# Kernel optimization log

Hardware: AMD Instinct MI355X
Metric: run time of the kernel (lower is better)

The kernel has to match this reference:

```python
import jax, jax.numpy as jnp
import numpy as np

DIM = 256
HEADS = 8
WIN = 64
SHIFT = 32
HIDDEN = 1024  # dim * mlp_ratio
EPS = 1e-5


def layernorm(x, g, b):
    mu = jnp.mean(x, axis=-1, keepdims=True)
    var = jnp.mean(jnp.square(x - mu), axis=-1, keepdims=True)
    return (x - mu) * jax.lax.rsqrt(var + EPS) * g + b


def setup_inputs() -> dict:
    key = jax.random.key(0)
    ks = jax.random.split(key, 12)
    B, L = 8, 16384
    s = lambda fan: 1.0 / np.sqrt(fan)
    return {
        "x": jax.random.normal(ks[0], (B, L, DIM), dtype=jnp.float32),
        "g1": jnp.ones((DIM,), jnp.float32),
        "b1": jnp.zeros((DIM,), jnp.float32),
        "qkv_w": jax.random.normal(ks[1], (DIM, 3 * DIM), jnp.float32) * s(DIM),
        "qkv_b": jnp.zeros((3 * DIM,), jnp.float32),
        "rpb_table": jax.random.normal(ks[2], (2 * WIN - 1, HEADS), jnp.float32) * 0.02,
        "proj_w": jax.random.normal(ks[3], (DIM, DIM), jnp.float32) * s(DIM),
        "proj_b": jnp.zeros((DIM,), jnp.float32),
        "g2": jnp.ones((DIM,), jnp.float32),
        "b2": jnp.zeros((DIM,), jnp.float32),
        "fc1_w": jax.random.normal(ks[4], (DIM, HIDDEN), jnp.float32) * s(DIM),
        "fc1_b": jnp.zeros((HIDDEN,), jnp.float32),
        "fc2_w": jax.random.normal(ks[5], (HIDDEN, DIM), jnp.float32) * s(HIDDEN),
        "fc2_b": jnp.zeros((DIM,), jnp.float32),
    }


def reference(x, g1, b1, qkv_w, qkv_b, rpb_table, proj_w, proj_b, g2, b2, fc1_w, fc1_b, fc2_w, fc2_b):
    B, L, C = x.shape
    hd = C // HEADS
    scale = hd ** (-0.5)

    shortcut = x
    xn = layernorm(x, g1, b1)

    # shift: roll left, zero wrapped-around tail (faithful to original in-place zeroing)
    shifted = jnp.roll(xn, -SHIFT, axis=1)
    shifted = shifted.at[:, -SHIFT:].set(0.0)

    nW = L // WIN
    xw = shifted.reshape(B * nW, WIN, C)

    # qkv projection
    qkv = xw @ qkv_w + qkv_b
    qkv = qkv.reshape(-1, WIN, 3, HEADS, hd).transpose(2, 0, 3, 1, 4)
    q, k, v = qkv[0], qkv[1], qkv[2]

    attn = jnp.einsum('bhnd,bhmd->bhnm', q * scale, k)

    idx = jnp.arange(WIN)
    rel = idx[:, None] - idx[None, :] + (WIN - 1)
    bias = rpb_table[rel].transpose(2, 0, 1)
    attn = attn + bias[None]

    attn = jax.nn.softmax(attn, axis=-1)
    out = jnp.einsum('bhnm,bhmd->bhnd', attn, v)
    out = out.transpose(0, 2, 1, 3).reshape(-1, WIN, C)
    out = out @ proj_w + proj_b

    # window reverse + unshift (zero wrapped head, faithful to original)
    xr = out.reshape(B, L, C)
    xr = jnp.roll(xr, SHIFT, axis=1)
    xr = xr.at[:, :SHIFT].set(0.0)

    x1 = shortcut + xr
    h = layernorm(x1, g2, b2)
    h = jax.nn.gelu(h @ fc1_w + fc1_b, approximate=False)
    h = h @ fc2_w + fc2_b
    return x1 + h
```

## Files before the change

### kernel.cpp

```cpp
#include <hip/hip_runtime.h>
#include <hip/hip_bf16.h>
#include <stdint.h>

#define LSEQ   16384
#define NBATCH 8
#define MROWS  (NBATCH*LSEQ)
#define CDIM   256
#define NHEADS 8
#define HDIM   32
#define NWIN   64
#define NSH    32
#define NHID   1024

typedef unsigned short u16;
typedef __attribute__((ext_vector_type(4))) float f32x4;
typedef __attribute__((ext_vector_type(8))) short s16x8;

__device__ __forceinline__ u16 f2bf(float f) {
  union { float f; unsigned u; } c; c.f = f;
  unsigned r = c.u + 0x7FFFu + ((c.u >> 16) & 1u);
  return (u16)(r >> 16);
}

__device__ __forceinline__ float gelu_fast(float v) {
  float t = v * v;
  float u2 = v * fmaf(t, 0.0713548162726f, 1.59576912161f);
  float e = __expf(u2);
  float r = __builtin_amdgcn_rcpf(e + 1.f);
  return fmaf(-v, r, v);
}

__global__ __launch_bounds__(256) void wtrans_kernel(const float* __restrict__ in,
                                                     u16* __restrict__ out, int K, int N) {
  __shared__ float tile[64][65];
  int k0 = blockIdx.x * 64, n0 = blockIdx.y * 64;
  int t = threadIdx.x;
  int r = t >> 4, cb = (t & 15) * 4;
#pragma unroll
  for (int p = 0; p < 4; ++p) {
    const float4 v = *(const float4*)(in + (size_t)(k0 + r + p*16) * N + n0 + cb);
    tile[r+p*16][cb+0] = v.x; tile[r+p*16][cb+1] = v.y;
    tile[r+p*16][cb+2] = v.z; tile[r+p*16][cb+3] = v.w;
  }
  __syncthreads();
#pragma unroll
  for (int p = 0; p < 4; ++p) {
    int nl = r + p*16;
    ushort4 o;
    o.x = f2bf(tile[cb+0][nl]); o.y = f2bf(tile[cb+1][nl]);
    o.z = f2bf(tile[cb+2][nl]); o.w = f2bf(tile[cb+3][nl]);
    *(ushort4*)(out + (size_t)(n0+nl)*K + k0 + cb) = o;
  }
}

__global__ __launch_bounds__(256) void ln_shift_kernel(const float* __restrict__ x,
                                                       const float* __restrict__ g,
                                                       const float* __restrict__ b,
                                                       u16* __restrict__ out) {
  int row  = blockIdx.x * 4 + (threadIdx.x >> 6);
  int lane = threadIdx.x & 63;
  u16* op = out + (size_t)row * CDIM + lane*4;
  int l  = row & (LSEQ-1);
  int ls = l + NSH;
  if (ls >= LSEQ) { *(ushort4*)op = make_ushort4(0,0,0,0); return; }
  const float4 v = *(const float4*)(x + ((size_t)(row - l) + ls) * CDIM + lane*4);
  float s  = v.x+v.y+v.z+v.w;
  float s2 = v.x*v.x + v.y*v.y + v.z*v.z + v.w*v.w;
#pragma unroll
  for (int m = 1; m < 64; m <<= 1) { s += __shfl_xor(s, m); s2 += __shfl_xor(s2, m); }
  float mean = s * (1.f/CDIM);
  float rs = rsqrtf(s2*(1.f/CDIM) - mean*mean + 1e-5f);
  const float4 gv = *(const float4*)(g + lane*4);
  const float4 bv = *(const float4*)(b + lane*4);
  ushort4 o;
  o.x = f2bf((v.x-mean)*rs*gv.x + bv.x);
  o.y = f2bf((v.y-mean)*rs*gv.y + bv.y);
  o.z = f2bf((v.z-mean)*rs*gv.z + bv.z);
  o.w = f2bf((v.w-mean)*rs*gv.w + bv.w);
  *(ushort4*)op = o;
}

template<int KDIM, int NDIM>
__global__ __launch_bounds__(256) void gemm_kernel(const u16* __restrict__ A,
                                                   const u16* __restrict__ BT,
                                                   const float* __restrict__ bias,
                                                   u16* __restrict__ Cout) {
  __shared__ __align__(16) u16 As[128*64];
  __shared__ __align__(16) u16 Bs[128*64];
  const int t = threadIdx.x, wave = t >> 6, lane = t & 63;
  constexpr int NT_N = NDIM / 128;
  constexpr int G = 32;
  const int bid = blockIdx.x;
  const int chunk = bid / (G * NT_N);
  const int rem = bid - chunk * (G * NT_N);
  const int tn = rem / G;
  const int tm = chunk * G + (rem - tn * G);
  f32x4 acc[4][4];
#pragma unroll
  for (int m = 0; m < 4; ++m)
#pragma unroll
    for (int n = 0; n < 4; ++n) acc[m][n] = (f32x4){0.f,0.f,0.f,0.f};

  const size_t Aoff = (size_t)tm * 128 * KDIM;
  const size_t Boff = (size_t)tn * 128 * KDIM;
  int rowS[4], kblkS[4];
#pragma unroll
  for (int p = 0; p < 4; ++p) {
    int i = p*256 + t; rowS[p] = i >> 3;
    kblkS[p] = ((i & 7) ^ (rowS[p] & 7)) * 8;
  }
  const int wr = (wave >> 1) * 64, wc = (wave & 1) * 64;

  for (int kt = 0; kt < KDIM/64; ++kt) {
    const int k0 = kt * 64;
#pragma unroll
    for (int p = 0; p < 4; ++p) {
      __builtin_amdgcn_global_load_lds(
        (const __attribute__((address_space(1))) void*)(A + Aoff + (size_t)rowS[p]*KDIM + k0 + kblkS[p]),
        (__attribute__((address_space(3))) void*)(As + (p*256 + wave*64)*8), 16, 0, 0);
      __builtin_amdgcn_global_load_lds(
        (const __attribute__((address_space(1))) void*)(BT + Boff + (size_t)rowS[p]*KDIM + k0 + kblkS[p]),
        (__attribute__((address_space(3))) void*)(Bs + (p*256 + wave*64)*8), 16, 0, 0);
    }
    asm volatile("s_waitcnt vmcnt(0)" ::: "memory");
    __syncthreads();
#pragma unroll
    for (int kk = 0; kk < 2; ++kk) {
      s16x8 af[4], bf[4];
#pragma unroll
      for (int m = 0; m < 4; ++m) {
        int r = wr + m*16 + (lane & 15);
        int slot = (kk*4 + (lane >> 4)) ^ (r & 7);
        af[m] = *(const s16x8*)&As[r*64 + slot*8];
      }
#pragma unroll
      for (int n = 0; n < 4; ++n) {
        int r = wc + n*16 + (lane & 15);
        int slot = (kk*4 + (lane >> 4)) ^ (r & 7);
        bf[n] = *(const s16x8*)&Bs[r*64 + slot*8];
      }
#pragma unroll
      for (int m = 0; m < 4; ++m)
#pragma unroll
        for (int n = 0; n < 4; ++n)
          acc[m][n] = __builtin_amdgcn_mfma_f32_16x16x32_bf16(bf[n], af[m], acc[m][n], 0, 0, 0);
    }
    __syncthreads();
  }

  const int g = lane >> 4, c0 = lane & 15;
  const size_t row0 = (size_t)tm*128 + wr;
  const int col0 = tn*128 + wc;
  float4 bvv[4];
#pragma unroll
  for (int n = 0; n < 4; ++n) bvv[n] = *(const float4*)(bias + col0 + n*16 + g*4);
#pragma unroll
  for (int m = 0; m < 4; ++m) {
    size_t R = row0 + m*16 + c0;
    u16* orow = Cout + R * NDIM + col0 + g*4;
#pragma unroll
    for (int n = 0; n < 4; ++n) {
      ushort4 o;
      o.x = f2bf(acc[m][n][0] + bvv[n].x);
      o.y = f2bf(acc[m][n][1] + bvv[n].y);
      o.z = f2bf(acc[m][n][2] + bvv[n].z);
      o.w = f2bf(acc[m][n][3] + bvv[n].w);
      *(ushort4*)(orow + n*16) = o;
    }
  }
}

__global__ __launch_bounds__(256) void proj_ln_kernel(const u16* __restrict__ A,
                                                      const u16* __restrict__ BT,
                                                      const float* __restrict__ bias,
                                                      const float* __restrict__ x,
                                                      const float* __restrict__ g2,
                                                      const float* __restrict__ b2,
                                                      float* __restrict__ out,
                                                      u16* __restrict__ ln_out) {
  __shared__ __align__(16) u16 As[64*64];
  __shared__ __align__(16) u16 Bs[256*64];
  const int t = threadIdx.x, wave = t >> 6, lane = t & 63;
  const int g = lane >> 4, c0 = lane & 15;
  const int row0 = blockIdx.x * 64;

  f32x4 acc[16];
#pragma unroll
  for (int n = 0; n < 16; ++n) acc[n] = (f32x4){0.f,0.f,0.f,0.f};

  for (int kt = 0; kt < 4; ++kt) {
    const int k0 = kt * 64;
#pragma unroll
    for (int p = 0; p < 2; ++p) {
      int i = p*256 + t;
      int r = i >> 3;
      int srow = row0 - NSH + r; if (srow < 0) srow = 0;
      int kb = ((i & 7) ^ (r & 7)) * 8;
      __builtin_amdgcn_global_load_lds(
        (const __attribute__((address_space(1))) void*)(A + (size_t)srow*CDIM + k0 + kb),
        (__attribute__((address_space(3))) void*)(As + i*8), 16, 0, 0);
    }
#pragma unroll
    for (int p = 0; p < 8; ++p) {
      int i = p*256 + t;
      int r = i >> 3;
      int kb = ((i & 7) ^ (r & 7)) * 8;
      __builtin_amdgcn_global_load_lds(
        (const __attribute__((address_space(1))) void*)(BT + (size_t)r*CDIM + k0 + kb),
        (__attribute__((address_space(3))) void*)(Bs + i*8), 16, 0, 0);
    }
    asm volatile("s_waitcnt vmcnt(0)" ::: "memory");
    __syncthreads();
#pragma unroll
    for (int kk = 0; kk < 2; ++kk) {
      const int ar = wave*16 + c0;
      s16x8 af = *(const s16x8*)&As[ar*64 + (((kk*4 + g) ^ (ar & 7)) * 8)];
#pragma unroll
      for (int nn = 0; nn < 4; ++nn) {
        s16x8 bf[4];
#pragma unroll
        for (int q = 0; q < 4; ++q) {
          int rn = (nn*4 + q)*16 + c0;
          bf[q] = *(const s16x8*)&Bs[rn*64 + (((kk*4 + g) ^ (rn & 7)) * 8)];
        }
#pragma unroll
        for (int q = 0; q < 4; ++q)
          acc[nn*4+q] = __builtin_amdgcn_mfma_f32_16x16x32_bf16(bf[q], af, acc[nn*4+q], 0, 0, 0);
      }
    }
    __syncthreads();
  }

  const int D = row0 + wave*16 + c0;
  const int l_d = D & (LSEQ-1);
  const bool addp = (l_d >= NSH);
  float s = 0.f, s2 = 0.f;
  f32x4 x1v[16];
#pragma unroll
  for (int n = 0; n < 16; ++n) {
    const int col = n*16 + g*4;
    const float4 xv = *(const float4*)(x + (size_t)D*CDIM + col);
    const float4 bv = *(const float4*)(bias + col);
    f32x4 v;
    v[0] = addp ? xv.x + acc[n][0] + bv.x : xv.x;
    v[1] = addp ? xv.y + acc[n][1] + bv.y : xv.y;
    v[2] = addp ? xv.z + acc[n][2] + bv.z : xv.z;
    v[3] = addp ? xv.w + acc[n][3] + bv.w : xv.w;
    *(f32x4*)(out + (size_t)D*CDIM + col) = v;
    x1v[n] = v;
    s  += v[0]+v[1]+v[2]+v[3];
    s2 += v[0]*v[0]+v[1]*v[1]+v[2]*v[2]+v[3]*v[3];
  }
  s  += __shfl_xor(s, 16);  s  += __shfl_xor(s, 32);
  s2 += __shfl_xor(s2, 16); s2 += __shfl_xor(s2, 32);
  const float mean = s * (1.f/CDIM);
  const float rs = rsqrtf(s2*(1.f/CDIM) - mean*mean + 1e-5f);
#pragma unroll
  for (int n = 0; n < 16; ++n) {
    const int col = n*16 + g*4;
    const float4 gv = *(const float4*)(g2 + col);
    const float4 bv = *(const float4*)(b2 + col);
    ushort4 o;
    o.x = f2bf((x1v[n][0]-mean)*rs*gv.x + bv.x);
    o.y = f2bf((x1v[n][1]-mean)*rs*gv.y + bv.y);
    o.z = f2bf((x1v[n][2]-mean)*rs*gv.z + bv.z);
    o.w = f2bf((x1v[n][3]-mean)*rs*gv.w + bv.w);
    *(ushort4*)(ln_out + (size_t)D*CDIM + col) = o;
  }
}

__global__ __launch_bounds__(256) void mlp_kernel(const u16* __restrict__ A,
                                                  const u16* __restrict__ W1T,
                                                  const u16* __restrict__ W2T,
                                                  const float* __restrict__ b1,
                                                  const float* __restrict__ b2,
                                                  float* __restrict__ out) {
  __shared__ __align__(16) u16 Xs[64*256];
  __shared__ __align__(16) u16 Ws[256*64];
  __shared__ __align__(16) u16 Hs[64*128];
  const int t = threadIdx.x, wave = t >> 6, lane = t & 63;
  const int g = lane >> 4, c0 = lane & 15;
  const int row0 = blockIdx.x * 64;

#pragma unroll
  for (int p = 0; p < 8; ++p) {
    int i = p*256 + t, r = i >> 5, cb = i & 31;
    __builtin_amdgcn_global_load_lds(
      (const __attribute__((address_space(1))) void*)(A + (size_t)(row0 + r)*CDIM + ((cb ^ (r & 7))*8)),
      (__attribute__((address_space(3))) void*)(Xs + i*8), 16, 0, 0);
  }
  f32x4 acc2[4][4];
#pragma unroll
  for (int m = 0; m < 4; ++m)
#pragma unroll
    for (int n = 0; n < 4; ++n) acc2[m][n] = (f32x4){0.f,0.f,0.f,0.f};
  asm volatile("s_waitcnt vmcnt(0)" ::: "memory");
  __syncthreads();

#pragma unroll 1
  for (int hc = 0; hc < 8; ++hc) {
    f32x4 acc1[4][2];
#pragma unroll
    for (int m = 0; m < 4; ++m) { acc1[m][0] = (f32x4){0.f,0.f,0.f,0.f}; acc1[m][1] = (f32x4){0.f,0.f,0.f,0.f}; }
#pragma unroll
    for (int kt = 0; kt < 4; ++kt) {
#pragma unroll
      for (int p = 0; p < 4; ++p) {
        int i = p*256 + t, r = i >> 3, cb = i & 7;
        __builtin_amdgcn_global_load_lds(
          (const __attribute__((address_space(1))) void*)(W1T + (size_t)(hc*128 + r)*256 + kt*64 + ((cb ^ (r & 7))*8)),
          (__attribute__((address_space(3))) void*)(Ws + i*8), 16, 0, 0);
      }
      asm volatile("s_waitcnt vmcnt(0)" ::: "memory");
      __syncthreads();
#pragma unroll
      for (int kk = 0; kk < 2; ++kk) {
        s16x8 af[4], bf[2];
        const int q = kt*2 + kk;
#pragma unroll
        for (int m = 0; m < 4; ++m) {
          int r = m*16 + c0;
          af[m] = *(const s16x8*)&Xs[r*256 + (((q*4 + g) ^ (r & 7))*8)];
        }
#pragma unroll
        for (int n = 0; n < 2; ++n) {
          int rw = wave*32 + n*16 + c0;
          bf[n] = *(const s16x8*)&Ws[rw*64 + (((kk*4 + g) ^ (rw & 7))*8)];
        }
#pragma unroll
        for (int m = 0; m < 4; ++m)
#pragma unroll
          for (int n = 0; n < 2; ++n)
            acc1[m][n] = __builtin_amdgcn_mfma_f32_16x16x32_bf16(bf[n], af[m], acc1[m][n], 0, 0, 0);
      }
      __syncthreads();
    }
    {
      float4 b1v[2];
#pragma unroll
      for (int n = 0; n < 2; ++n) b1v[n] = *(const float4*)(b1 + hc*128 + wave*32 + n*16 + g*4);
#pragma unroll
      for (int m = 0; m < 4; ++m) {
        int r = m*16 + c0;
#pragma unroll
        for (int n = 0; n < 2; ++n) {
          ushort4 o;
          o.x = f2bf(gelu_fast(acc1[m][n][0] + b1v[n].x));
          o.y = f2bf(gelu_fast(acc1[m][n][1] + b1v[n].y));
          o.z = f2bf(gelu_fast(acc1[m][n][2] + b1v[n].z));
          o.w = f2bf(gelu_fast(acc1[m][n][3] + b1v[n].w));
          int colb = wave*4 + n*2 + (g >> 1);
          *(ushort4*)((char*)Hs + r*256 + ((colb ^ (r & 7)) << 4) + (g & 1)*8) = o;
        }
      }
    }
    __syncthreads();
#pragma unroll
    for (int kt2 = 0; kt2 < 2; ++kt2) {
#pragma unroll
      for (int p = 0; p < 8; ++p) {
        int i = p*256 + t, r = i >> 3, cb = i & 7;
        __builtin_amdgcn_global_load_lds(
          (const __attribute__((address_space(1))) void*)(W2T + (size_t)r*NHID + hc*128 + kt2*64 + ((cb ^ (r & 7))*8)),
          (__attribute__((address_space(3))) void*)(Ws + i*8), 16, 0, 0);
      }
      asm volatile("s_waitcnt vmcnt(0)" ::: "memory");
      __syncthreads();
#pragma unroll
      for (int kk = 0; kk < 2; ++kk) {
        s16x8 af[4], bf[4];
        const int s2 = kt2*2 + kk;
#pragma unroll
        for (int m = 0; m < 4; ++m) {
          int r = m*16 + c0;
          af[m] = *(const s16x8*)&Hs[r*128 + (((s2*4 + g) ^ (r & 7))*8)];
        }
#pragma unroll
        for (int n = 0; n < 4; ++n) {
          int rw = wave*64 + n*16 + c0;
          bf[n] = *(const s16x8*)&Ws[rw*64 + (((kk*4 + g) ^ (rw & 7))*8)];
        }
#pragma unroll
        for (int m = 0; m < 4; ++m)
#pragma unroll
          for (int n = 0; n < 4; ++n)
            acc2[m][n] = __builtin_amdgcn_mfma_f32_16x16x32_bf16(bf[n], af[m], acc2[m][n], 0, 0, 0);
      }
      __syncthreads();
    }
  }
  float4 b2v[4];
#pragma unroll
  for (int n = 0; n < 4; ++n) b2v[n] = *(const float4*)(b2 + wave*64 + n*16 + g*4);
#pragma unroll
  for (int m = 0; m < 4; ++m) {
    size_t base = (size_t)(row0 + m*16 + c0)*CDIM + wave*64 + g*4;
#pragma unroll
    for (int n = 0; n < 4; ++n) {
      float4 rv = *(const float4*)(out + base + n*16);
      float4 o;
      o.x = rv.x + acc2[m][n][0] + b2v[n].x;
      o.y = rv.y + acc2[m][n][1] + b2v[n].y;
      o.z = rv.z + acc2[m][n][2] + b2v[n].z;
      o.w = rv.w + acc2[m][n][3] + b2v[n].w;
      *(float4*)(out + base + n*16) = o;
    }
  }
}

__global__ __launch_bounds__(256) void attn_kernel(const u16* __restrict__ qkv,
                                                   const float* __restrict__ rpb,
                                                   u16* __restrict__ out) {
  __shared__ __align__(16) u16 VT[NHEADS*HDIM*NWIN];
  __shared__ __align__(16) u16 Pl[4*NWIN*NWIN];
  __shared__ float biasl[NHEADS][128];
  const int t = threadIdx.x, wave = t >> 6, lane = t & 63;
  const int g = lane >> 4, c0 = lane & 15;
  const size_t rowbase = (size_t)blockIdx.x * NWIN;

  for (int e = t; e < NHEADS*128; e += 256) {
    int h = e >> 7, i = e & 127;
    biasl[h][i] = (i < 2*NWIN-1) ? rpb[i*NHEADS + h] : 0.f;
  }
  {
    int cA = t >> 5;
    int inner = t & 31;
    int hh = inner >> 2, d0 = (inner & 3) * 8;
#pragma unroll
    for (int p = 0; p < 8; ++p) {
      int c = p*8 + cA;
      s16x8 v = *(const s16x8*)&qkv[(rowbase + c)*768 + 512 + hh*32 + d0];
#pragma unroll
      for (int j = 0; j < 8; ++j) {
        int d = d0 + j;
        int slot = (c >> 3) ^ (d & 7) ^ hh;
        *(u16*)((char*)VT + hh*4096 + d*128 + slot*16 + (c & 7)*2) = (u16)v[j];
      }
    }
  }
  __syncthreads();

  const float scale = 0.17677669529663687f;
#pragma unroll 1
  for (int rep = 0; rep < 2; ++rep) {
    const int h = wave*2 + rep;
    s16x8 qf[4], kf[4];
#pragma unroll
    for (int m = 0; m < 4; ++m)
      qf[m] = *(const s16x8*)&qkv[(rowbase + m*16 + c0)*768 + h*32 + g*8];
#pragma unroll
    for (int n = 0; n < 4; ++n)
      kf[n] = *(const s16x8*)&qkv[(rowbase + n*16 + c0)*768 + 256 + h*32 + g*8];
    f32x4 sa[4][4];
#pragma unroll
    for (int m = 0; m < 4; ++m)
#pragma unroll
      for (int n = 0; n < 4; ++n) sa[m][n] = (f32x4){0.f,0.f,0.f,0.f};
#pragma unroll
    for (int m = 0; m < 4; ++m)
#pragma unroll
      for (int n = 0; n < 4; ++n)
        sa[m][n] = __builtin_amdgcn_mfma_f32_16x16x32_bf16(qf[m], kf[n], sa[m][n], 0, 0, 0);
#pragma unroll
    for (int m = 0; m < 4; ++m)
#pragma unroll
      for (int n = 0; n < 4; ++n) {
        int idx0 = (m-n)*16 + 4*g - c0 + 63;
#pragma unroll
        for (int j = 0; j < 4; ++j)
          sa[m][n][j] = sa[m][n][j]*scale + biasl[h][idx0 + j];
      }
    float rm[4][4], rsum[4][4];
#pragma unroll
    for (int m = 0; m < 4; ++m)
#pragma unroll
      for (int j = 0; j < 4; ++j) {
        float mx = fmaxf(fmaxf(sa[m][0][j], sa[m][1][j]), fmaxf(sa[m][2][j], sa[m][3][j]));
        mx = fmaxf(mx, __shfl_xor(mx, 1));
        mx = fmaxf(mx, __shfl_xor(mx, 2));
        mx = fmaxf(mx, __shfl_xor(mx, 4));
        mx = fmaxf(mx, __shfl_xor(mx, 8));
        rm[m][j] = mx;
      }
#pragma unroll
    for (int m = 0; m < 4; ++m)
#pragma unroll
      for (int n = 0; n < 4; ++n)
#pragma unroll
        for (int j = 0; j < 4; ++j)
          sa[m][n][j] = __expf(sa[m][n][j] - rm[m][j]);
#pragma unroll
    for (int m = 0; m < 4; ++m)
#pragma unroll
      for (int j = 0; j < 4; ++j) {
        float s = sa[m][0][j] + sa[m][1][j] + sa[m][2][j] + sa[m][3][j];
        s += __shfl_xor(s, 1);
        s += __shfl_xor(s, 2);
        s += __shfl_xor(s, 4);
        s += __shfl_xor(s, 8);
        rsum[m][j] = 1.f / s;
      }
    asm volatile("s_waitcnt lgkmcnt(0)" ::: "memory");
#pragma unroll
    for (int m = 0; m < 4; ++m)
#pragma unroll
      for (int n = 0; n < 4; ++n)
#pragma unroll
        for (int j = 0; j < 4; ++j) {
          int r = m*16 + 4*g + j, c = n*16 + c0;
          *(u16*)((char*)Pl + wave*8192 + r*128 + (((c>>3)^(r&7))*16) + (c&7)*2)
            = f2bf(sa[m][n][j] * rsum[m][j]);
        }
    asm volatile("s_waitcnt lgkmcnt(0)" ::: "memory");
    __builtin_amdgcn_sched_barrier(0);
    f32x4 oa[4][2];
#pragma unroll
    for (int m = 0; m < 4; ++m) { oa[m][0] = (f32x4){0.f,0.f,0.f,0.f}; oa[m][1] = (f32x4){0.f,0.f,0.f,0.f}; }
#pragma unroll
    for (int kk = 0; kk < 2; ++kk) {
      s16x8 pa[4], vb[2];
#pragma unroll
      for (int m = 0; m < 4; ++m) {
        int r = m*16 + c0;
        int slot = (kk*4 + g) ^ (r & 7);
        pa[m] = *(const s16x8*)((const char*)Pl + wave*8192 + r*128 + slot*16);
      }
#pragma unroll
      for (int n = 0; n < 2; ++n) {
        int d = n*16 + c0;
        int slot = (kk*4 + g) ^ (d & 7) ^ h;
        vb[n] = *(const s16x8*)((const char*)VT + h*4096 + d*128 + slot*16);
      }
#pragma unroll
      for (int m = 0; m < 4; ++m)
#pragma unroll
        for (int n = 0; n < 2; ++n)
          oa[m][n] = __builtin_amdgcn_mfma_f32_16x16x32_bf16(vb[n], pa[m], oa[m][n], 0, 0, 0);
    }
#pragma unroll
    for (int m = 0; m < 4; ++m) {
      u16* op = out + (rowbase + m*16 + c0)*CDIM + h*32 + g*4;
#pragma unroll
      for (int n = 0; n < 2; ++n) {
        ushort4 o;
        o.x = f2bf(oa[m][n][0]); o.y = f2bf(oa[m][n][1]);
        o.z = f2bf(oa[m][n][2]); o.w = f2bf(oa[m][n][3]);
        *(ushort4*)(op + n*16) = o;
      }
    }
  }
}

extern "C" void kernel_launch(void* const* d_in, const int* in_sizes, int n_in,
                              void* d_out, int out_size, void* d_ws, size_t ws_size,
                              hipStream_t stream) {
  const float* x      = (const float*)d_in[0];
  const float* g1     = (const float*)d_in[1];
  const float* b1     = (const float*)d_in[2];
  const float* qkv_w  = (const float*)d_in[3];
  const float* qkv_b  = (const float*)d_in[4];
  const float* rpb    = (const float*)d_in[5];
  const float* proj_w = (const float*)d_in[6];
  const float* proj_b = (const float*)d_in[7];
  const float* g2     = (const float*)d_in[8];
  const float* b2     = (const float*)d_in[9];
  const float* fc1_w  = (const float*)d_in[10];
  const float* fc1_b  = (const float*)d_in[11];
  const float* fc2_w  = (const float*)d_in[12];
  const float* fc2_b  = (const float*)d_in[13];
  float* out = (float*)d_out;

  u16* R0     = (u16*)d_ws;
  u16* R1     = R0 + (size_t)MROWS*768;
  u16* qkvwT  = R1 + (size_t)MROWS*1024;
  u16* projwT = qkvwT + 768*256;
  u16* fc1wT  = projwT + 256*256;
  u16* fc2wT  = fc1wT + 1024*256;

  wtrans_kernel<<<dim3(4, 12), 256, 0, stream>>>(qkv_w, qkvwT, 256, 768);
  wtrans_kernel<<<dim3(4, 4),  256, 0, stream>>>(proj_w, projwT, 256, 256);
  wtrans_kernel<<<dim3(4, 16), 256, 0, stream>>>(fc1_w, fc1wT, 256, 1024);
  wtrans_kernel<<<dim3(16, 4), 256, 0, stream>>>(fc2_w, fc2wT, 1024, 256);

  constexpr int NT_M = MROWS/128;
  ln_shift_kernel<<<MROWS/4, 256, 0, stream>>>(x, g1, b1, R1);
  gemm_kernel<256, 768><<<NT_M*6, 256, 0, stream>>>(R1, qkvwT, qkv_b, R0);
  attn_kernel<<<MROWS/NWIN, 256, 0, stream>>>(R0, rpb, R1);
  proj_ln_kernel<<<MROWS/64, 256, 0, stream>>>(R1, projwT, proj_b, x, g2, b2, out, R0);
  mlp_kernel<<<MROWS/64, 256, 0, stream>>>(R0, fc1wT, fc2wT, fc1_b, fc2_b, out);
}
```

Before: 642.8 us.

## Restructure fused MLP into 64-wide hidden chunks with overlapped W2 loads

The fused MLP kernel now walks the hidden dimension in 16 chunks of 64 instead of 8 chunks of 128. Each chunk loads the full 256-deep W1 slice in a single transfer rather than four. The W2 slice load is issued before the GELU epilogue, so it overlaps with the Hs writes, and the initial X load wait is merged into the first weight wait. The aim is fewer barriers and waits per chunk and some hiding of global-to-LDS latency, at the cost of smaller MFMA tiles per wave in the first GEMM and twice as many outer iterations.

```diff
diff --git a/kernel.cpp b/kernel.cpp
--- a/kernel.cpp
+++ b/kernel.cpp
@@ -276,8 +276,8 @@
                                                   const float* __restrict__ b2,
                                                   float* __restrict__ out) {
   __shared__ __align__(16) u16 Xs[64*256];
-  __shared__ __align__(16) u16 Ws[256*64];
-  __shared__ __align__(16) u16 Hs[64*128];
+  __shared__ __align__(16) u16 Ws[64*256];
+  __shared__ __align__(16) u16 Hs[64*64];
   const int t = threadIdx.x, wave = t >> 6, lane = t & 63;
   const int g = lane >> 4, c0 = lane & 15;
   const int row0 = blockIdx.x * 64;
@@ -294,100 +294,79 @@
   for (int m = 0; m < 4; ++m)
 #pragma unroll
     for (int n = 0; n < 4; ++n) acc2[m][n] = (f32x4){0.f,0.f,0.f,0.f};
-  asm volatile("s_waitcnt vmcnt(0)" ::: "memory");
-  __syncthreads();
 
 #pragma unroll 1
-  for (int hc = 0; hc < 8; ++hc) {
-    f32x4 acc1[4][2];
-#pragma unroll
-    for (int m = 0; m < 4; ++m) { acc1[m][0] = (f32x4){0.f,0.f,0.f,0.f}; acc1[m][1] = (f32x4){0.f,0.f,0.f,0.f}; }
-#pragma unroll
-    for (int kt = 0; kt < 4; ++kt) {
-#pragma unroll
-      for (int p = 0; p < 4; ++p) {
-        int i = p*256 + t, r = i >> 3, cb = i & 7;
-        __builtin_amdgcn_global_load_lds(
-          (const __attribute__((address_space(1))) void*)(W1T + (size_t)(hc*128 + r)*256 + kt*64 + ((cb ^ (r & 7))*8)),
-          (__attribute__((address_space(3))) void*)(Ws + i*8), 16, 0, 0);
-      }
-      asm volatile("s_waitcnt vmcnt(0)" ::: "memory");
-      __syncthreads();
-#pragma unroll
-      for (int kk = 0; kk < 2; ++kk) {
-        s16x8 af[4], bf[2];
-        const int q = kt*2 + kk;
-#pragma unroll
-        for (int m = 0; m < 4; ++m) {
-          int r = m*16 + c0;
-          af[m] = *(const s16x8*)&Xs[r*256 + (((q*4 + g) ^ (r & 7))*8)];
-        }
-#pragma unroll
-        for (int n = 0; n < 2; ++n) {
-          int rw = wave*32 + n*16 + c0;
-          bf[n] = *(const s16x8*)&Ws[rw*64 + (((kk*4 + g) ^ (rw & 7))*8)];
-        }
-#pragma unroll
-        for (int m = 0; m < 4; ++m)
-#pragma unroll
-          for (int n = 0; n < 2; ++n)
-            acc1[m][n] = __builtin_amdgcn_mfma_f32_16x16x32_bf16(bf[n], af[m], acc1[m][n], 0, 0, 0);
-      }
-      __syncthreads();
-    }
-    {
-      float4 b1v[2];
-#pragma unroll
-      for (int n = 0; n < 2; ++n) b1v[n] = *(const float4*)(b1 + hc*128 + wave*32 + n*16 + g*4);
+  for (int hc2 = 0; hc2 < 16; ++hc2) {
+#pragma unroll
+    for (int p = 0; p < 8; ++p) {
+      int i = p*256 + t, r = i >> 5, cb = i & 31;
+      __builtin_amdgcn_global_load_lds(
+        (const __attribute__((address_space(1))) void*)(W1T + (size_t)(hc2*64 + r)*256 + ((cb ^ (r & 7))*8)),
+        (__attribute__((address_space(3))) void*)(Ws + i*8), 16, 0, 0);
+    }
+    asm volatile("s_waitcnt vmcnt(0)" ::: "memory");
+    __syncthreads();
+    f32x4 acc1[4];
+#pragma unroll
+    for (int m = 0; m < 4; ++m) acc1[m] = (f32x4){0.f,0.f,0.f,0.f};
+#pragma unroll
+    for (int q = 0; q < 8; ++q) {
+      s16x8 af[4];
 #pragma unroll
       for (int m = 0; m < 4; ++m) {
         int r = m*16 + c0;
-#pragma unroll
-        for (int n = 0; n < 2; ++n) {
-          ushort4 o;
-          o.x = f2bf(gelu_fast(acc1[m][n][0] + b1v[n].x));
-          o.y = f2bf(gelu_fast(acc1[m][n][1] + b1v[n].y));
-          o.z = f2bf(gelu_fast(acc1[m][n][2] + b1v[n].z));
-          o.w = f2bf(gelu_fast(acc1[m][n][3] + b1v[n].w));
-          int colb = wave*4 + n*2 + (g >> 1);
-          *(ushort4*)((char*)Hs + r*256 + ((colb ^ (r & 7)) << 4) + (g & 1)*8) = o;
-        }
-      }
-    }
-    __syncthreads();
-#pragma unroll
-    for (int kt2 = 0; kt2 < 2; ++kt2) {
-#pragma unroll
-      for (int p = 0; p < 8; ++p) {
-        int i = p*256 + t, r = i >> 3, cb = i & 7;
-        __builtin_amdgcn_global_load_lds(
-          (const __attribute__((address_space(1))) void*)(W2T + (size_t)r*NHID + hc*128 + kt2*64 + ((cb ^ (r & 7))*8)),
-          (__attribute__((address_space(3))) void*)(Ws + i*8), 16, 0, 0);
-      }
-      asm volatile("s_waitcnt vmcnt(0)" ::: "memory");
-      __syncthreads();
-#pragma unroll
-      for (int kk = 0; kk < 2; ++kk) {
-        s16x8 af[4], bf[4];
-        const int s2 = kt2*2 + kk;
-#pragma unroll
-        for (int m = 0; m < 4; ++m) {
-          int r = m*16 + c0;
-          af[m] = *(const s16x8*)&Hs[r*128 + (((s2*4 + g) ^ (r & 7))*8)];
-        }
-#pragma unroll
-        for (int n = 0; n < 4; ++n) {
-          int rw = wave*64 + n*16 + c0;
-          bf[n] = *(const s16x8*)&Ws[rw*64 + (((kk*4 + g) ^ (rw & 7))*8)];
-        }
-#pragma unroll
-        for (int m = 0; m < 4; ++m)
-#pragma unroll
-          for (int n = 0; n < 4; ++n)
-            acc2[m][n] = __builtin_amdgcn_mfma_f32_16x16x32_bf16(bf[n], af[m], acc2[m][n], 0, 0, 0);
-      }
-      __syncthreads();
-    }
+        af[m] = *(const s16x8*)&Xs[r*256 + (((q*4 + g) ^ (r & 7))*8)];
+      }
+      int rw = wave*16 + c0;
+      s16x8 bf = *(const s16x8*)&Ws[rw*256 + (((q*4 + g) ^ (rw & 7))*8)];
+#pragma unroll
+      for (int m = 0; m < 4; ++m)
+        acc1[m] = __builtin_amdgcn_mfma_f32_16x16x32_bf16(bf, af[m], acc1[m], 0, 0, 0);
+    }
+    __syncthreads();
+#pragma unroll
+    for (int p = 0; p < 8; ++p) {
+      int i = p*256 + t, r = i >> 3, cb = i & 7;
+      __builtin_amdgcn_global_load_lds(
+        (const __attribute__((address_space(1))) void*)(W2T + (size_t)r*NHID + hc2*64 + ((cb ^ (r & 7))*8)),
+        (__attribute__((address_space(3))) void*)(Ws + i*8), 16, 0, 0);
+    }
+    {
+      const float4 bv = *(const float4*)(b1 + hc2*64 + wave*16 + g*4);
+#pragma unroll
+      for (int m = 0; m < 4; ++m) {
+        int r = m*16 + c0;
+        ushort4 o;
+        o.x = f2bf(gelu_fast(acc1[m][0] + bv.x));
+        o.y = f2bf(gelu_fast(acc1[m][1] + bv.y));
+        o.z = f2bf(gelu_fast(acc1[m][2] + bv.z));
+        o.w = f2bf(gelu_fast(acc1[m][3] + bv.w));
+        int colb = wave*2 + (g >> 1);
+        *(ushort4*)((char*)Hs + r*128 + ((colb ^ (r & 7)) << 4) + (g & 1)*8) = o;
+      }
+    }
+    asm volatile("s_waitcnt vmcnt(0)" ::: "memory");
+    __syncthreads();
+#pragma unroll
+    for (int kk = 0; kk < 2; ++kk) {
+      s16x8 af[4], bf[4];
+#pragma unroll
+      for (int m = 0; m < 4; ++m) {
+        int r = m*16 + c0;
+        af[m] = *(const s16x8*)&Hs[r*64 + (((kk*4 + g) ^ (r & 7))*8)];
+      }
+#pragma unroll
+      for (int n = 0; n < 4; ++n) {
+        int rw = wave*64 + n*16 + c0;
+        bf[n] = *(const s16x8*)&Ws[rw*64 + (((kk*4 + g) ^ (rw & 7))*8)];
+      }
+#pragma unroll
+      for (int m = 0; m < 4; ++m)
+#pragma unroll
+        for (int n = 0; n < 4; ++n)
+          acc2[m][n] = __builtin_amdgcn_mfma_f32_16x16x32_bf16(bf[n], af[m], acc2[m][n], 0, 0, 0);
+    }
+    __syncthreads();
   }
   float4 b2v[4];
 #pragma unroll
```

After: 620.2 us, median of 2. -3.5%, faster.

## Restructure MLP fc1 tiling to 2x2 wave grid with larger K-chunks and overlapped W2 loads

Applied to the files above, without the earlier changes.

In the fused MLP kernel, fc1 now uses a 2x2 wave grid (32 rows by 64 hidden columns per wave) and stages W1 in two 128-wide K chunks instead of four 64-wide ones. This halves the number of barrier/wait rounds and improves operand reuse per LDS read. The first W2 tile load is issued before the GELU epilogue so its latency overlaps with the activation math. The initial X-load wait is folded into the first W1 wait. The cost is a larger LDS footprint for the weight tile (still 32KB), fewer X-operand reuses per wave, and more manually unrolled code.

```diff
diff --git a/kernel.cpp b/kernel.cpp
--- a/kernel.cpp
+++ b/kernel.cpp
@@ -276,11 +276,12 @@
                                                   const float* __restrict__ b2,
                                                   float* __restrict__ out) {
   __shared__ __align__(16) u16 Xs[64*256];
-  __shared__ __align__(16) u16 Ws[256*64];
+  __shared__ __align__(16) u16 Ws[128*128];
   __shared__ __align__(16) u16 Hs[64*128];
   const int t = threadIdx.x, wave = t >> 6, lane = t & 63;
   const int g = lane >> 4, c0 = lane & 15;
   const int row0 = blockIdx.x * 64;
+  const int rblk = (wave >> 1) * 32, hblk = (wave & 1) * 64;
 
 #pragma unroll
   for (int p = 0; p < 8; ++p) {
@@ -294,100 +295,126 @@
   for (int m = 0; m < 4; ++m)
 #pragma unroll
     for (int n = 0; n < 4; ++n) acc2[m][n] = (f32x4){0.f,0.f,0.f,0.f};
-  asm volatile("s_waitcnt vmcnt(0)" ::: "memory");
-  __syncthreads();
 
 #pragma unroll 1
   for (int hc = 0; hc < 8; ++hc) {
-    f32x4 acc1[4][2];
-#pragma unroll
-    for (int m = 0; m < 4; ++m) { acc1[m][0] = (f32x4){0.f,0.f,0.f,0.f}; acc1[m][1] = (f32x4){0.f,0.f,0.f,0.f}; }
-#pragma unroll
-    for (int kt = 0; kt < 4; ++kt) {
-#pragma unroll
-      for (int p = 0; p < 4; ++p) {
-        int i = p*256 + t, r = i >> 3, cb = i & 7;
+    const int hcb = hc * 128;
+    f32x4 acc1[2][4];
+#pragma unroll
+    for (int mm = 0; mm < 2; ++mm)
+#pragma unroll
+      for (int nn = 0; nn < 4; ++nn) acc1[mm][nn] = (f32x4){0.f,0.f,0.f,0.f};
+#pragma unroll
+    for (int kh = 0; kh < 2; ++kh) {
+#pragma unroll
+      for (int p = 0; p < 8; ++p) {
+        int i = p*256 + t, r = i >> 4, cb = i & 15;
         __builtin_amdgcn_global_load_lds(
-          (const __attribute__((address_space(1))) void*)(W1T + (size_t)(hc*128 + r)*256 + kt*64 + ((cb ^ (r & 7))*8)),
+          (const __attribute__((address_space(1))) void*)(W1T + (size_t)(hcb + r)*256 + kh*128 + ((cb ^ (r & 7))*8)),
           (__attribute__((address_space(3))) void*)(Ws + i*8), 16, 0, 0);
       }
       asm volatile("s_waitcnt vmcnt(0)" ::: "memory");
       __syncthreads();
 #pragma unroll
-      for (int kk = 0; kk < 2; ++kk) {
-        s16x8 af[4], bf[2];
-        const int q = kt*2 + kk;
-#pragma unroll
-        for (int m = 0; m < 4; ++m) {
-          int r = m*16 + c0;
-          af[m] = *(const s16x8*)&Xs[r*256 + (((q*4 + g) ^ (r & 7))*8)];
+      for (int q = 0; q < 4; ++q) {
+        s16x8 af[2], bf[4];
+#pragma unroll
+        for (int mm = 0; mm < 2; ++mm) {
+          int r = rblk + mm*16 + c0;
+          af[mm] = *(const s16x8*)&Xs[r*256 + (((kh*16 + q*4 + g) ^ (r & 7))*8)];
         }
 #pragma unroll
-        for (int n = 0; n < 2; ++n) {
-          int rw = wave*32 + n*16 + c0;
-          bf[n] = *(const s16x8*)&Ws[rw*64 + (((kk*4 + g) ^ (rw & 7))*8)];
+        for (int nn = 0; nn < 4; ++nn) {
+          int rw = hblk + nn*16 + c0;
+          bf[nn] = *(const s16x8*)&Ws[rw*128 + (((q*4 + g) ^ (rw & 7))*8)];
         }
 #pragma unroll
-        for (int m = 0; m < 4; ++m)
-#pragma unroll
-          for (int n = 0; n < 2; ++n)
-            acc1[m][n] = __builtin_amdgcn_mfma_f32_16x16x32_bf16(bf[n], af[m], acc1[m][n], 0, 0, 0);
+        for (int mm = 0; mm < 2; ++mm)
+#pragma unroll
+          for (int nn = 0; nn < 4; ++nn)
+            acc1[mm][nn] = __builtin_amdgcn_mfma_f32_16x16x32_bf16(bf[nn], af[mm], acc1[mm][nn], 0, 0, 0);
       }
       __syncthreads();
     }
+#pragma unroll
+    for (int p = 0; p < 8; ++p) {
+      int i = p*256 + t, r = i >> 3, cb = i & 7;
+      __builtin_amdgcn_global_load_lds(
+        (const __attribute__((address_space(1))) void*)(W2T + (size_t)r*NHID + hcb + ((cb ^ (r & 7))*8)),
+        (__attribute__((address_space(3))) void*)(Ws + i*8), 16, 0, 0);
+    }
     {
-      float4 b1v[2];
-#pragma unroll
-      for (int n = 0; n < 2; ++n) b1v[n] = *(const float4*)(b1 + hc*128 + wave*32 + n*16 + g*4);
+      float4 b1v[4];
+#pragma unroll
+      for (int nn = 0; nn < 4; ++nn) b1v[nn] = *(const float4*)(b1 + hcb + hblk + nn*16 + g*4);
+#pragma unroll
+      for (int mm = 0; mm < 2; ++mm) {
+        int r = rblk + mm*16 + c0;
+#pragma unroll
+        for (int nn = 0; nn < 4; ++nn) {
+          ushort4 o;
+          o.x = f2bf(gelu_fast(acc1[mm][nn][0] + b1v[nn].x));
+          o.y = f2bf(gelu_fast(acc1[mm][nn][1] + b1v[nn].y));
+          o.z = f2bf(gelu_fast(acc1[mm][nn][2] + b1v[nn].z));
+          o.w = f2bf(gelu_fast(acc1[mm][nn][3] + b1v[nn].w));
+          int colb = (hblk >> 3) + nn*2 + (g >> 1);
+          *(ushort4*)((char*)Hs + r*256 + ((colb ^ (r & 7)) << 4) + (g & 1)*8) = o;
+        }
+      }
+    }
+    asm volatile("s_waitcnt vmcnt(0)" ::: "memory");
+    __syncthreads();
+#pragma unroll
+    for (int kk = 0; kk < 2; ++kk) {
+      s16x8 af[4], bf[4];
+      const int s2 = kk;
 #pragma unroll
       for (int m = 0; m < 4; ++m) {
         int r = m*16 + c0;
-#pragma unroll
-        for (int n = 0; n < 2; ++n) {
-          ushort4 o;
-          o.x = f2bf(gelu_fast(acc1[m][n][0] + b1v[n].x));
-          o.y = f2bf(gelu_fast(acc1[m][n][1] + b1v[n].y));
-          o.z = f2bf(gelu_fast(acc1[m][n][2] + b1v[n].z));
-          o.w = f2bf(gelu_fast(acc1[m][n][3] + b1v[n].w));
-          int colb = wave*4 + n*2 + (g >> 1);
-          *(ushort4*)((char*)Hs + r*256 + ((colb ^ (r & 7)) << 4) + (g & 1)*8) = o;
-        }
-      }
-    }
-    __syncthreads();
-#pragma unroll
-    for (int kt2 = 0; kt2 < 2; ++kt2) {
-#pragma unroll
-      for (int p = 0; p < 8; ++p) {
-        int i = p*256 + t, r = i >> 3, cb = i & 7;
-        __builtin_amdgcn_global_load_lds(
-          (const __attribute__((address_space(1))) void*)(W2T + (size_t)r*NHID + hc*128 + kt2*64 + ((cb ^ (r & 7))*8)),
-          (__attribute__((address_space(3))) void*)(Ws + i*8), 16, 0, 0);
-      }
-      asm volatile("s_waitcnt vmcnt(0)" ::: "memory");
-      __syncthreads();
-#pragma unroll
-      for (int kk = 0; kk < 2; ++kk) {
-        s16x8 af[4], bf[4];
-        const int s2 = kt2*2 + kk;
-#pragma unroll
-        for (int m = 0; m < 4; ++m) {
-          int r = m*16 + c0;
-          af[m] = *(const s16x8*)&Hs[r*128 + (((s2*4 + g) ^ (r & 7))*8)];
-        }
-#pragma unroll
-        for (int n = 0; n < 4; ++n) {
-          int rw = wave*64 + n*16 + c0;
-          bf[n] = *(const s16x8*)&Ws[rw*64 + (((kk*4 + g) ^ (rw & 7))*8)];
-        }
-#pragma unroll
-        for (int m = 0; m < 4; ++m)
-#pragma unroll
-          for (int n = 0; n < 4; ++n)
-            acc2[m][n] = __builtin_amdgcn_mfma_f32_16x16x32_bf16(bf[n], af[m], acc2[m][n], 0, 0, 0);
-      }
-      __syncthreads();
-    }
+        af[m] = *(const s16x8*)&Hs[r*128 + (((s2*4 + g) ^ (r & 7))*8)];
+      }
+#pragma unroll
+      for (int n = 0; n < 4; ++n) {
+        int rw = wave*64 + n*16 + c0;
+        bf[n] = *(const s16x8*)&Ws[rw*64 + (((kk*4 + g) ^ (rw & 7))*8)];
+      }
+#pragma unroll
+      for (int m = 0; m < 4; ++m)
+#pragma unroll
+        for (int n = 0; n < 4; ++n)
+          acc2[m][n] = __builtin_amdgcn_mfma_f32_16x16x32_bf16(bf[n], af[m], acc2[m][n], 0, 0, 0);
+    }
+    __syncthreads();
+#pragma unroll
+    for (int p = 0; p < 8; ++p) {
+      int i = p*256 + t, r = i >> 3, cb = i & 7;
+      __builtin_amdgcn_global_load_lds(
+        (const __attribute__((address_space(1))) void*)(W2T + (size_t)r*NHID + hcb + 64 + ((cb ^ (r & 7))*8)),
+        (__attribute__((address_space(3))) void*)(Ws + i*8), 16, 0, 0);
+    }
+    asm volatile("s_waitcnt vmcnt(0)" ::: "memory");
+    __syncthreads();
+#pragma unroll
+    for (int kk = 0; kk < 2; ++kk) {
+      s16x8 af[4], bf[4];
+      const int s2 = 2 + kk;
+#pragma unroll
+      for (int m = 0; m < 4; ++m) {
+        int r = m*16 + c0;
+        af[m] = *(const s16x8*)&Hs[r*128 + (((s2*4 + g) ^ (r & 7))*8)];
+      }
+#pragma unroll
+      for (int n = 0; n < 4; ++n) {
+        int rw = wave*64 + n*16 + c0;
+        bf[n] = *(const s16x8*)&Ws[rw*64 + (((kk*4 + g) ^ (rw & 7))*8)];
+      }
+#pragma unroll
+      for (int m = 0; m < 4; ++m)
+#pragma unroll
+        for (int n = 0; n < 4; ++n)
+          acc2[m][n] = __builtin_amdgcn_mfma_f32_16x16x32_bf16(bf[n], af[m], acc2[m][n], 0, 0, 0);
+    }
+    __syncthreads();
   }
   float4 b2v[4];
 #pragma unroll
```

New measurement: 631.2 us. Within noise of the previous version (-1.8%).
